# Optimization experiments

Hardware: AMD Instinct MI355X
Metric: run time of the kernel (lower is better)

## Reference

```python
import jax, jax.numpy as jnp
import numpy as np

B, V, K, C = 32, 65536, 8, 3


def setup_inputs() -> dict:
    key = jax.random.key(0)
    k1, k2, k3, k4 = jax.random.split(key, 4)
    out = jax.random.normal(k1, (B, V, C), dtype=jnp.float32)
    tgt = jax.random.normal(k2, (B, V, C), dtype=jnp.float32)
    neighbor_idxs = jax.random.randint(k3, (V, K), 0, V, dtype=jnp.int32)
    # Laplacian weights: each row sums to -1 (lap = x - weighted mean of neighbors)
    w = jax.random.uniform(k4, (V, K), dtype=jnp.float32) + 1e-3
    neighbor_weights = -w / jnp.sum(w, axis=-1, keepdims=True)
    return {
        "out": out,
        "tgt": tgt,
        "neighbor_idxs": neighbor_idxs,
        "neighbor_weights": neighbor_weights,
    }


def _compute_laplacian(x, neighbor_idxs, neighbor_weights):
    # x: [B, V, C]; gather -> [B, V, K, C]; weighted sum over K; residual add
    gathered = x[:, neighbor_idxs]                       # [B, V, K, C]
    return x + jnp.sum(gathered * neighbor_weights[None, :, :, None], axis=2)


def reference(out, tgt, neighbor_idxs, neighbor_weights):
    lap_out = _compute_laplacian(out, neighbor_idxs, neighbor_weights)
    lap_tgt = _compute_laplacian(tgt, neighbor_idxs, neighbor_weights)
    return (lap_out - lap_tgt) ** 2
```

## Files before the change

kernel.cpp:

```cpp
#include <hip/hip_runtime.h>

#define BB 32
#define VV 65536
#define KK 8
#define CC 3

constexpr int TV   = 32;
constexpr int ROW  = BB * CC;
constexpr int PROW = ROW + 1;
constexpr int TILE_ELEMS = TV * ROW;
constexpr int ROWU = ROW / 2;

__device__ __forceinline__ unsigned int f2bf(float f) {
  unsigned int u = __float_as_uint(f);
  u += 0x7FFFu + ((u >> 16) & 1u);
  return u >> 16;
}
__device__ __forceinline__ float bflo(unsigned int u) { return __uint_as_float(u << 16); }
__device__ __forceinline__ float bfhi(unsigned int u) { return __uint_as_float(u & 0xFFFF0000u); }

struct U3 { unsigned int x, y, z; };

__global__ __launch_bounds__(256) void lap_pass1_transpose_sub(
    const float* __restrict__ outp, const float* __restrict__ tgtp,
    unsigned int* __restrict__ dt) {
  __shared__ float tile[TV * PROW];
  const int t  = threadIdx.x;
  const int v0 = blockIdx.x * TV;

  const float4* o4 = (const float4*)outp;
  const float4* t4 = (const float4*)tgtp;
  const int src_base4 = (v0 * CC) >> 2;
  #pragma unroll
  for (int l4 = t; l4 < TILE_ELEMS / 4; l4 += 256) {
    int b  = l4 / (TV * CC / 4);
    int j4 = l4 - b * (TV * CC / 4);
    int src = b * (VV * CC / 4) + src_base4 + j4;
    float4 a = o4[src];
    float4 g = t4[src];
    float dv[4] = {a.x - g.x, a.y - g.y, a.z - g.z, a.w - g.w};
    int j = 4 * j4;
    #pragma unroll
    for (int q = 0; q < 4; q++) {
      int jj = j + q;
      int vrel = jj / CC, c = jj - vrel * CC;
      tile[vrel * PROW + b * CC + c] = dv[q];
    }
  }
  __syncthreads();

  uint4* dst = (uint4*)(dt + (size_t)v0 * ROWU);
  #pragma unroll
  for (int i8 = t; i8 < TILE_ELEMS / 8; i8 += 256) {
    int e = i8 * 8;
    int vrel = e / ROW, r = e - vrel * ROW;
    const float* p = &tile[vrel * PROW + r];
    uint4 o;
    o.x = f2bf(p[0]) | (f2bf(p[1]) << 16);
    o.y = f2bf(p[2]) | (f2bf(p[3]) << 16);
    o.z = f2bf(p[4]) | (f2bf(p[5]) << 16);
    o.w = f2bf(p[6]) | (f2bf(p[7]) << 16);
    dst[i8] = o;
  }
}

__global__ __launch_bounds__(256) void lap_pass2_gather(
    const unsigned int* __restrict__ dt, const int* __restrict__ nidx,
    const float* __restrict__ nw, float* __restrict__ res) {
  __shared__ float rtile[TV * PROW];
  __shared__ int   idx_s[TV * KK];
  __shared__ float w_s[TV * KK];
  const int t  = threadIdx.x;
  const int v0 = blockIdx.x * TV;

  if (t < TV * KK) {
    idx_s[t] = nidx[v0 * KK + t];
    w_s[t]   = nw[v0 * KK + t];
  }
  __syncthreads();

  const int g = t >> 4;
  const int l = t & 15;
  #pragma unroll
  for (int i = 0; i < TV / 16; i++) {
    const int vrel = i * 16 + g;
    const int v    = v0 + vrel;

    const int4*   ip = (const int4*)&idx_s[vrel * KK];
    const float4* wp = (const float4*)&w_s[vrel * KK];
    int4   ia = ip[0], ib = ip[1];
    float4 wa = wp[0], wb = wp[1];
    int   nbk[KK] = {ia.x, ia.y, ia.z, ia.w, ib.x, ib.y, ib.z, ib.w};
    float wk[KK]  = {wa.x, wa.y, wa.z, wa.w, wb.x, wb.y, wb.z, wb.w};

    U3 s = *(const U3*)(dt + (size_t)v * ROWU + 3 * l);
    float x0 = bflo(s.x), y0 = bfhi(s.x), z0 = bflo(s.y);
    float x1 = bfhi(s.y), y1 = bflo(s.z), z1 = bfhi(s.z);

    #pragma unroll
    for (int k = 0; k < KK; k++) {
      U3 u = *(const U3*)(dt + (size_t)nbk[k] * ROWU + 3 * l);
      const float wt = wk[k];
      x0 = fmaf(wt, bflo(u.x), x0);
      y0 = fmaf(wt, bfhi(u.x), y0);
      z0 = fmaf(wt, bflo(u.y), z0);
      x1 = fmaf(wt, bfhi(u.y), x1);
      y1 = fmaf(wt, bflo(u.z), y1);
      z1 = fmaf(wt, bfhi(u.z), z1);
    }
    float* rp = &rtile[vrel * PROW + 6 * l];
    rp[0] = x0 * x0; rp[1] = y0 * y0; rp[2] = z0 * z0;
    rp[3] = x1 * x1; rp[4] = y1 * y1; rp[5] = z1 * z1;
  }
  __syncthreads();

  float4* r4 = (float4*)res;
  const int dst_base4 = (v0 * CC) >> 2;
  #pragma unroll
  for (int l4 = t; l4 < TILE_ELEMS / 4; l4 += 256) {
    int b  = l4 / (TV * CC / 4);
    int j4 = l4 - b * (TV * CC / 4);
    int j  = 4 * j4;
    float tmp[4];
    #pragma unroll
    for (int q = 0; q < 4; q++) {
      int jj = j + q;
      int vrel = jj / CC, c = jj - vrel * CC;
      tmp[q] = rtile[vrel * PROW + b * CC + c];
    }
    r4[b * (VV * CC / 4) + dst_base4 + j4] = make_float4(tmp[0], tmp[1], tmp[2], tmp[3]);
  }
}

__global__ __launch_bounds__(256) void lap_fused_fallback(
    const float* __restrict__ outp, const float* __restrict__ tgtp,
    const int* __restrict__ nidx, const float* __restrict__ nw,
    float* __restrict__ res) {
  int tid = blockIdx.x * 256 + threadIdx.x;
  if (tid >= BB * VV) return;
  int v = tid & (VV - 1);
  int b = tid >> 16;
  float ax = 0.f, ay = 0.f, az = 0.f;
  #pragma unroll
  for (int k = 0; k < KK; k++) {
    int   nb = nidx[v * KK + k];
    float wt = nw[v * KK + k];
    const float* po = outp + ((size_t)b * VV + nb) * CC;
    const float* pt = tgtp + ((size_t)b * VV + nb) * CC;
    ax = fmaf(wt, po[0] - pt[0], ax);
    ay = fmaf(wt, po[1] - pt[1], ay);
    az = fmaf(wt, po[2] - pt[2], az);
  }
  const float* so = outp + (size_t)tid * CC;
  const float* st = tgtp + (size_t)tid * CC;
  float dx = so[0] - st[0] + ax;
  float dy = so[1] - st[1] + ay;
  float dz = so[2] - st[2] + az;
  float* rp = res + (size_t)tid * CC;
  rp[0] = dx * dx; rp[1] = dy * dy; rp[2] = dz * dz;
}

extern "C" void kernel_launch(void* const* d_in, const int* in_sizes, int n_in,
                              void* d_out, int out_size, void* d_ws, size_t ws_size,
                              hipStream_t stream) {
  const float* outp = (const float*)d_in[0];
  const float* tgtp = (const float*)d_in[1];
  const int*   nidx = (const int*)d_in[2];
  const float* nw   = (const float*)d_in[3];
  float* res = (float*)d_out;

  const size_t dt_bytes = (size_t)VV * ROW * 2;
  if (ws_size >= dt_bytes) {
    unsigned int* dt = (unsigned int*)d_ws;
    lap_pass1_transpose_sub<<<VV / TV, 256, 0, stream>>>(outp, tgtp, dt);
    lap_pass2_gather<<<VV / TV, 256, 0, stream>>>(dt, nidx, nw, res);
  } else {
    lap_fused_fallback<<<(BB * VV) / 256, 256, 0, stream>>>(outp, tgtp, nidx, nw, res);
  }
}
```

Baseline: 115.6 us.

## Split bf16 diff buffer into batch chunks and gather per chunk

The transposed bf16 difference buffer is reorganised into 8 batch chunks of 4 batches each, so each vertex row per chunk is 24 bytes. The gather kernel now runs one block per (chunk, 128-vertex tile), with two threads per vertex instead of sixteen. Pass 1 also uses 64-vertex tiles. The goal is a smaller per-chunk gather working set with better cache locality, at the cost of narrower 24-byte gathers that waste more of each cache line, and neighbor index and weight data reloaded once per chunk.

```diff
diff --git a/kernel.cpp b/kernel.cpp
--- a/kernel.cpp
+++ b/kernel.cpp
@@ -5,11 +5,18 @@
 #define KK 8
 #define CC 3
 
-constexpr int TV   = 32;
-constexpr int ROW  = BB * CC;
-constexpr int PROW = ROW + 1;
-constexpr int TILE_ELEMS = TV * ROW;
-constexpr int ROWU = ROW / 2;
+constexpr int NCHUNK = 8;
+constexpr int CB     = BB / NCHUNK;
+constexpr int CROW   = CB * CC;
+constexpr int CROWU  = CROW / 2;
+
+constexpr int TV1   = 64;
+constexpr int ROW   = BB * CC;
+constexpr int PROW1 = ROW + 1;
+constexpr int T1ELEMS = TV1 * ROW;
+
+constexpr int TV2   = 128;
+constexpr int PROW2 = CROW + 1;
 
 __device__ __forceinline__ unsigned int f2bf(float f) {
   unsigned int u = __float_as_uint(f);
@@ -24,17 +31,17 @@
 __global__ __launch_bounds__(256) void lap_pass1_transpose_sub(
     const float* __restrict__ outp, const float* __restrict__ tgtp,
     unsigned int* __restrict__ dt) {
-  __shared__ float tile[TV * PROW];
+  __shared__ float tile[TV1 * PROW1];
   const int t  = threadIdx.x;
-  const int v0 = blockIdx.x * TV;
+  const int v0 = blockIdx.x * TV1;
 
   const float4* o4 = (const float4*)outp;
   const float4* t4 = (const float4*)tgtp;
   const int src_base4 = (v0 * CC) >> 2;
   #pragma unroll
-  for (int l4 = t; l4 < TILE_ELEMS / 4; l4 += 256) {
-    int b  = l4 / (TV * CC / 4);
-    int j4 = l4 - b * (TV * CC / 4);
+  for (int l4 = t; l4 < T1ELEMS / 4; l4 += 256) {
+    int b  = l4 / (TV1 * CC / 4);
+    int j4 = l4 - b * (TV1 * CC / 4);
     int src = b * (VV * CC / 4) + src_base4 + j4;
     float4 a = o4[src];
     float4 g = t4[src];
@@ -44,91 +51,95 @@
     for (int q = 0; q < 4; q++) {
       int jj = j + q;
       int vrel = jj / CC, c = jj - vrel * CC;
-      tile[vrel * PROW + b * CC + c] = dv[q];
+      tile[vrel * PROW1 + b * CC + c] = dv[q];
     }
   }
   __syncthreads();
 
-  uint4* dst = (uint4*)(dt + (size_t)v0 * ROWU);
   #pragma unroll
-  for (int i8 = t; i8 < TILE_ELEMS / 8; i8 += 256) {
-    int e = i8 * 8;
-    int vrel = e / ROW, r = e - vrel * ROW;
-    const float* p = &tile[vrel * PROW + r];
+  for (int u = t; u < NCHUNK * (TV1 * CROWU / 4); u += 256) {
+    int chunk = u / (TV1 * CROWU / 4);
+    int i16   = u - chunk * (TV1 * CROWU / 4);
+    int E = i16 * 8;
+    unsigned int w[8];
+    #pragma unroll
+    for (int q = 0; q < 8; q++) {
+      int ee = E + q;
+      int vrel = ee / CROW, jj = ee - vrel * CROW;
+      w[q] = f2bf(tile[vrel * PROW1 + chunk * CROW + jj]);
+    }
     uint4 o;
-    o.x = f2bf(p[0]) | (f2bf(p[1]) << 16);
-    o.y = f2bf(p[2]) | (f2bf(p[3]) << 16);
-    o.z = f2bf(p[4]) | (f2bf(p[5]) << 16);
-    o.w = f2bf(p[6]) | (f2bf(p[7]) << 16);
-    dst[i8] = o;
+    o.x = w[0] | (w[1] << 16);
+    o.y = w[2] | (w[3] << 16);
+    o.z = w[4] | (w[5] << 16);
+    o.w = w[6] | (w[7] << 16);
+    uint4* dst = (uint4*)(dt + (size_t)chunk * (VV * CROWU) + (size_t)v0 * CROWU);
+    dst[i16] = o;
   }
 }
 
 __global__ __launch_bounds__(256) void lap_pass2_gather(
     const unsigned int* __restrict__ dt, const int* __restrict__ nidx,
     const float* __restrict__ nw, float* __restrict__ res) {
-  __shared__ float rtile[TV * PROW];
-  __shared__ int   idx_s[TV * KK];
-  __shared__ float w_s[TV * KK];
-  const int t  = threadIdx.x;
-  const int v0 = blockIdx.x * TV;
+  __shared__ float rtile[TV2 * PROW2];
+  __shared__ int   idx_s[TV2 * KK];
+  __shared__ float w_s[TV2 * KK];
+  const int t     = threadIdx.x;
+  const int chunk = blockIdx.x & (NCHUNK - 1);
+  const int v0    = (blockIdx.x >> 3) * TV2;
 
-  if (t < TV * KK) {
-    idx_s[t] = nidx[v0 * KK + t];
-    w_s[t]   = nw[v0 * KK + t];
-  }
+  ((int4*)idx_s)[t]  = ((const int4*)(nidx + (size_t)v0 * KK))[t];
+  ((float4*)w_s)[t]  = ((const float4*)(nw + (size_t)v0 * KK))[t];
   __syncthreads();
 
-  const int g = t >> 4;
-  const int l = t & 15;
+  const unsigned int* dtc = dt + (size_t)chunk * (VV * CROWU);
+  const int vrel = t >> 1;
+  const int l    = t & 1;
+  const int v    = v0 + vrel;
+
+  const int4*   ip = (const int4*)&idx_s[vrel * KK];
+  const float4* wp = (const float4*)&w_s[vrel * KK];
+  int4   ia = ip[0], ib = ip[1];
+  float4 wa = wp[0], wb = wp[1];
+  int   nbk[KK] = {ia.x, ia.y, ia.z, ia.w, ib.x, ib.y, ib.z, ib.w};
+  float wk[KK]  = {wa.x, wa.y, wa.z, wa.w, wb.x, wb.y, wb.z, wb.w};
+
+  U3 s = *(const U3*)(dtc + (size_t)v * CROWU + 3 * l);
+  float x0 = bflo(s.x), y0 = bfhi(s.x), z0 = bflo(s.y);
+  float x1 = bfhi(s.y), y1 = bflo(s.z), z1 = bfhi(s.z);
+
   #pragma unroll
-  for (int i = 0; i < TV / 16; i++) {
-    const int vrel = i * 16 + g;
-    const int v    = v0 + vrel;
-
-    const int4*   ip = (const int4*)&idx_s[vrel * KK];
-    const float4* wp = (const float4*)&w_s[vrel * KK];
-    int4   ia = ip[0], ib = ip[1];
-    float4 wa = wp[0], wb = wp[1];
-    int   nbk[KK] = {ia.x, ia.y, ia.z, ia.w, ib.x, ib.y, ib.z, ib.w};
-    float wk[KK]  = {wa.x, wa.y, wa.z, wa.w, wb.x, wb.y, wb.z, wb.w};
-
-    U3 s = *(const U3*)(dt + (size_t)v * ROWU + 3 * l);
-    float x0 = bflo(s.x), y0 = bfhi(s.x), z0 = bflo(s.y);
-    float x1 = bfhi(s.y), y1 = bflo(s.z), z1 = bfhi(s.z);
-
-    #pragma unroll
-    for (int k = 0; k < KK; k++) {
-      U3 u = *(const U3*)(dt + (size_t)nbk[k] * ROWU + 3 * l);
-      const float wt = wk[k];
-      x0 = fmaf(wt, bflo(u.x), x0);
-      y0 = fmaf(wt, bfhi(u.x), y0);
-      z0 = fmaf(wt, bflo(u.y), z0);
-      x1 = fmaf(wt, bfhi(u.y), x1);
-      y1 = fmaf(wt, bflo(u.z), y1);
-      z1 = fmaf(wt, bfhi(u.z), z1);
-    }
-    float* rp = &rtile[vrel * PROW + 6 * l];
-    rp[0] = x0 * x0; rp[1] = y0 * y0; rp[2] = z0 * z0;
-    rp[3] = x1 * x1; rp[4] = y1 * y1; rp[5] = z1 * z1;
+  for (int k = 0; k < KK; k++) {
+    U3 u = *(const U3*)(dtc + (size_t)nbk[k] * CROWU + 3 * l);
+    const float wt = wk[k];
+    x0 = fmaf(wt, bflo(u.x), x0);
+    y0 = fmaf(wt, bfhi(u.x), y0);
+    z0 = fmaf(wt, bflo(u.y), z0);
+    x1 = fmaf(wt, bfhi(u.y), x1);
+    y1 = fmaf(wt, bflo(u.z), y1);
+    z1 = fmaf(wt, bfhi(u.z), z1);
   }
+  float* rp = &rtile[vrel * PROW2 + 6 * l];
+  rp[0] = x0 * x0; rp[1] = y0 * y0; rp[2] = z0 * z0;
+  rp[3] = x1 * x1; rp[4] = y1 * y1; rp[5] = z1 * z1;
   __syncthreads();
 
   float4* r4 = (float4*)res;
   const int dst_base4 = (v0 * CC) >> 2;
   #pragma unroll
-  for (int l4 = t; l4 < TILE_ELEMS / 4; l4 += 256) {
-    int b  = l4 / (TV * CC / 4);
-    int j4 = l4 - b * (TV * CC / 4);
+  for (int l4 = t; l4 < CB * (TV2 * CC / 4); l4 += 256) {
+    int b  = l4 / (TV2 * CC / 4);
+    int j4 = l4 - b * (TV2 * CC / 4);
+    int bg = chunk * CB + b;
     int j  = 4 * j4;
     float tmp[4];
     #pragma unroll
     for (int q = 0; q < 4; q++) {
       int jj = j + q;
-      int vrel = jj / CC, c = jj - vrel * CC;
-      tmp[q] = rtile[vrel * PROW + b * CC + c];
+      int vr = jj / CC, c = jj - vr * CC;
+      tmp[q] = rtile[vr * PROW2 + b * CC + c];
     }
-    r4[b * (VV * CC / 4) + dst_base4 + j4] = make_float4(tmp[0], tmp[1], tmp[2], tmp[3]);
+    r4[bg * (VV * CC / 4) + dst_base4 + j4] = make_float4(tmp[0], tmp[1], tmp[2], tmp[3]);
   }
 }
 
@@ -172,8 +183,8 @@
   const size_t dt_bytes = (size_t)VV * ROW * 2;
   if (ws_size >= dt_bytes) {
     unsigned int* dt = (unsigned int*)d_ws;
-    lap_pass1_transpose_sub<<<VV / TV, 256, 0, stream>>>(outp, tgtp, dt);
-    lap_pass2_gather<<<VV / TV, 256, 0, stream>>>(dt, nidx, nw, res);
+    lap_pass1_transpose_sub<<<VV / TV1, 256, 0, stream>>>(outp, tgtp, dt);
+    lap_pass2_gather<<<NCHUNK * (VV / TV2), 256, 0, stream>>>(dt, nidx, nw, res);
   } else {
     lap_fused_fallback<<<(BB * VV) / 256, 256, 0, stream>>>(outp, tgtp, nidx, nw, res);
   }
```

New measurement: 120.9 us. 4.6% more time.
